# Kernel tuning notes

Measured on AMD Instinct MI355X. Metric: run time of the kernel, lower is better.

Reference implementation:

```python
import jax, jax.numpy as jnp
import numpy as np

B, K, D = 512, 20, 256


def _build_adjs(K):
    def tri(N):
        a = np.zeros((N, N), np.int32)
        a[0, 1] = a[1, 0] = 1
        a[0, 2] = a[2, 0] = 1
        a[1, 2] = a[2, 1] = 1
        return a
    adj1 = tri(3)
    adj2 = tri(3 + 3 * K)
    adj3 = tri(3 + 6 * K)
    for i in range(K):
        for c in range(3):
            adj2[c, 3 + c * K + i] = adj2[3 + c * K + i, c] = 2
            adj3[c, 3 + c * K + i] = adj3[3 + c * K + i, c] = 2
            adj3[c, 3 + 3 * K + c * K + i] = adj3[3 + 3 * K + c * K + i, c] = 3
    return jnp.asarray(adj1), jnp.asarray(adj2), jnp.asarray(adj3)

ADJ1, ADJ2, ADJ3 = _build_adjs(K)


def _rgat(h, adj, W, a_src, a_dst):
    # h: [B,N,F]; adj: [N,N] int relation labels (0 = no edge);
    # W: [R,F,E] per-relation projection; a_src/a_dst: [R,E] attention vecs.
    R = W.shape[0]
    Wh = jnp.einsum('bnf,rfe->brne', h, W)                      # [B,R,N,E]
    e = jax.nn.leaky_relu(
        jnp.einsum('brne,re->brn', Wh, a_src)[..., :, None]
        + jnp.einsum('brne,re->brn', Wh, a_dst)[..., None, :],
        negative_slope=0.2)                                     # [B,R,N,N]
    rel = jnp.arange(1, R + 1, dtype=jnp.int32)
    mask = (adj[None, :, :] == rel[:, None, None])[None]        # [1,R,N,N]
    alpha = jnp.where(mask, jax.nn.softmax(jnp.where(mask, e, -1e9), axis=-1), 0.0)
    return jax.nn.elu(jnp.einsum('brnm,brme->bne', alpha, Wh))  # [B,N,E]


def setup_inputs():
    key = jax.random.key(0)
    ks = jax.random.split(key, 40)
    n = lambda i, shp: jax.random.normal(ks[i], shp, dtype=jnp.float32)
    w = lambda i, shp: 0.02 * jax.random.normal(ks[i], shp, dtype=jnp.float32)
    inp = {
        'scene_tv': n(0, (B, 1, 1024)), 'face_tv': n(1, (B, 1, 1024)), 'text_tv': n(2, (B, 1, 2048)),
        'scene_refs': n(3, (B, K, 1024)), 'face_refs': n(4, (B, K, 1024)), 'text_refs': n(5, (B, K, 2048)),
        'scene_ra': n(6, (B, K, 1024)), 'face_ra': n(7, (B, K, 1024)), 'text_ra': n(8, (B, K, 1024)),
        'Ws1': w(9, (1024, D)), 'bs1': jnp.zeros((D,), jnp.float32),
        'Wf1': w(10, (1024, D)), 'bf1': jnp.zeros((D,), jnp.float32),
        'Wt1': w(11, (2048, D)), 'bt1': jnp.zeros((D,), jnp.float32),
        'G1W': w(12, (1, D, D)), 'G1as': w(13, (1, D)), 'G1ad': w(14, (1, D)),
        'Ws2': w(15, (1024, D)), 'bs2': jnp.zeros((D,), jnp.float32),
        'Wf2': w(16, (1024, D)), 'bf2': jnp.zeros((D,), jnp.float32),
        'Wt2': w(17, (2048, D)), 'bt2': jnp.zeros((D,), jnp.float32),
        'G2W': w(18, (2, D, D)), 'G2as': w(19, (2, D)), 'G2ad': w(20, (2, D)),
        'Ws3': w(21, (1024, D)), 'bs3': jnp.zeros((D,), jnp.float32),
        'Wf3': w(22, (1024, D)), 'bf3': jnp.zeros((D,), jnp.float32),
        'Wt3': w(23, (1024, D)), 'bt3': jnp.zeros((D,), jnp.float32),
        'G3W': w(24, (3, D, D)), 'G3as': w(25, (3, D)), 'G3ad': w(26, (3, D)),
    }
    return inp


def reference(scene_tv, face_tv, text_tv, scene_refs, face_refs, text_refs,
              scene_ra, face_ra, text_ra,
              Ws1, bs1, Wf1, bf1, Wt1, bt1, G1W, G1as, G1ad,
              Ws2, bs2, Wf2, bf2, Wt2, bt2, G2W, G2as, G2ad,
              Ws3, bs3, Wf3, bf3, Wt3, bt3, G3W, G3as, G3ad):
    # Stage 1: Basic_Emotion_Graph (3 nodes, 1 relation type)
    nodes1 = jnp.concatenate([scene_tv @ Ws1 + bs1,
                              face_tv @ Wf1 + bf1,
                              text_tv @ Wt1 + bt1], axis=1)      # [B,3,D]
    g1 = _rgat(nodes1, ADJ1, G1W, G1as, G1ad)
    # Stage 2: Indirect_Emotion_Extended_Graph (3+3K nodes, 2 relation types)
    nodes2 = jnp.concatenate([g1,
                              scene_refs @ Ws2 + bs2,
                              face_refs @ Wf2 + bf2,
                              text_refs @ Wt2 + bt2], axis=1)    # [B,3+3K,D]
    g2 = _rgat(nodes2, ADJ2, G2W, G2as, G2ad)
    # Stage 3: Direct_Emotion_Extended_Graph (3+6K nodes, 3 relation types)
    nodes3 = jnp.concatenate([g2,
                              scene_ra @ Ws3 + bs3,
                              face_ra @ Wf3 + bf3,
                              text_ra @ Wt3 + bt3], axis=1)      # [B,3+6K,D]
    return _rgat(nodes3, ADJ3, G3W, G3as, G3ad)
```

## Files before the change

### kernel.cpp

```cpp
#include <hip/hip_runtime.h>
#include <hip/hip_bf16.h>
#include <math.h>

typedef __bf16 bf16_t;
typedef __bf16 bf16x8 __attribute__((ext_vector_type(8)));
typedef __bf16 bf16x4 __attribute__((ext_vector_type(4)));
typedef float  floatx4 __attribute__((ext_vector_type(4)));

#define NB 512
#define DI 256

__device__ __forceinline__ float lrelu_f(float x){ return x >= 0.f ? x : 0.2f*x; }
__device__ __forceinline__ float elu_f(float x){ return x > 0.f ? x : expm1f(x); }

__global__ __launch_bounds__(256)
void detect_k(const void* __restrict__ probe, int* __restrict__ flag)
{
    __shared__ int cnt_s;
    if (threadIdx.x == 0) cnt_s = 0;
    __syncthreads();
    const unsigned short* u = (const unsigned short*)probe;
    int c = 0;
    for (int i = threadIdx.x; i < 16384; i += 256) {
        int e = (u[i] >> 7) & 0xFF;
        if (e >= 0x90) c++;
    }
    atomicAdd(&cnt_s, c);
    __syncthreads();
    if (threadIdx.x == 0) *flag = (cnt_s > 64) ? 1 : 0;
}

struct SCEnt { const void* s; bf16_t* d; int n; };
struct SCArgs { SCEnt e[16]; int cnt; };

__global__ __launch_bounds__(256)
void smallconv_k(SCArgs a, const int* __restrict__ flag)
{
    int isf = *flag;
    for (int k = 0; k < a.cnt; ++k) {
        int n = a.e[k].n;
        for (int i = threadIdx.x + blockIdx.x * 256; i < n; i += gridDim.x * 256) {
            float v = isf ? ((const float*)a.e[k].s)[i]
                          : (float)((const bf16_t*)a.e[k].s)[i];
            a.e[k].d[i] = (bf16_t)v;
        }
    }
}

struct TDesc { const void* W; size_t eoff; bf16_t* WT; int K; int tstart; };
struct TArgs { TDesc d[15]; int nd; };

__global__ __launch_bounds__(256)
void transpose_multi_k(TArgs ta, const int* __restrict__ flagp)
{
    __shared__ bf16_t tile[32][33];
    const int isf = *flagp;
    const int bx = blockIdx.x;
    int di = 0;
    while (di + 1 < ta.nd && bx >= ta.d[di + 1].tstart) ++di;
    const void* Wbase = ta.d[di].W;
    const size_t eoff = ta.d[di].eoff;
    bf16_t* WT        = ta.d[di].WT;
    const int K       = ta.d[di].K;
    const int ti      = bx - ta.d[di].tstart;
    const int tk      = K >> 5;
    const int kb      = (ti % tk) * 32;
    const int nb      = (ti / tk) * 32;
    const int tx = threadIdx.x & 31, ty = threadIdx.x >> 5;
    #pragma unroll
    for (int rr = 0; rr < 4; ++rr) {
        int r = ty + rr * 8;
        size_t idx = eoff + (size_t)(kb + r) * 256 + nb + tx;
        tile[r][tx] = isf ? (bf16_t)((const float*)Wbase)[idx]
                          : ((const bf16_t*)Wbase)[idx];
    }
    __syncthreads();
    #pragma unroll
    for (int rr = 0; rr < 4; ++rr) {
        int r = ty + rr * 8;
        WT[(size_t)(nb + r) * K + kb + tx] = tile[tx][r];
    }
}

#define BM 64
#define BN 64
#define BK 32
#define LST 40

struct GDesc {
    const void* A; const bf16_t* WT; const bf16_t* bias; bf16_t* out;
    int Kin, in_stride_b, in_off, rows_pb, a_is_ext, out_stride_b, out_off, mb_start;
};
struct GArgs { GDesc d[9]; int nd; };

__global__ __launch_bounds__(256)
void gemm_multi_k(GArgs ga, const int* __restrict__ flagp)
{
    __shared__ bf16_t As[BM * LST];
    __shared__ bf16_t Bs[BN * LST];

    const int bx = blockIdx.x;
    int di = 0;
    while (di + 1 < ga.nd && bx >= ga.d[di + 1].mb_start) ++di;

    const void*   A        = ga.d[di].A;
    const bf16_t* WT       = ga.d[di].WT;
    const bf16_t* bias     = ga.d[di].bias;
    bf16_t*       out      = ga.d[di].out;
    const int Kin          = ga.d[di].Kin;
    const int in_stride_b  = ga.d[di].in_stride_b;
    const int in_off       = ga.d[di].in_off;
    const int rows_pb      = ga.d[di].rows_pb;
    const int out_stride_b = ga.d[di].out_stride_b;
    const int out_off      = ga.d[di].out_off;
    const int a_fp32 = ga.d[di].a_is_ext ? *flagp : 0;

    const int t  = threadIdx.x;
    const int m0 = (bx - ga.d[di].mb_start) * BM;
    const int n0 = blockIdx.y * BN;

    const int s_row = t >> 2;
    const int s_col = (t & 3) * 8;

    const int g_row = m0 + s_row;
    const int b_idx = g_row / rows_pb;
    const int i_idx = g_row - b_idx * rows_pb;
    const size_t a_base = (size_t)(b_idx * in_stride_b + in_off + i_idx) * Kin + s_col;
    const bf16_t* w_ptr = WT + (size_t)(n0 + s_row) * Kin + s_col;

    const int wave = t >> 6;
    const int lane = t & 63;
    const int wr = (wave >> 1) * 32;
    const int wc = (wave & 1) * 32;
    const int lm = lane & 15;
    const int lk = (lane >> 4) * 8;

    floatx4 acc[2][2] = {};

    for (int kk = 0; kk < Kin; kk += BK) {
        bf16x8 av;
        if (a_fp32) {
            const float* ap = (const float*)A + a_base + kk;
            float4 f0 = *(const float4*)ap;
            float4 f1 = *(const float4*)(ap + 4);
            av[0] = (bf16_t)f0.x; av[1] = (bf16_t)f0.y;
            av[2] = (bf16_t)f0.z; av[3] = (bf16_t)f0.w;
            av[4] = (bf16_t)f1.x; av[5] = (bf16_t)f1.y;
            av[6] = (bf16_t)f1.z; av[7] = (bf16_t)f1.w;
        } else {
            av = *(const bf16x8*)((const bf16_t*)A + a_base + kk);
        }
        bf16x8 wv = *(const bf16x8*)(w_ptr + kk);
        *(bf16x8*)(&As[s_row * LST + s_col]) = av;
        *(bf16x8*)(&Bs[s_row * LST + s_col]) = wv;
        __syncthreads();

        bf16x8 af0 = *(const bf16x8*)(&As[(wr      + lm) * LST + lk]);
        bf16x8 af1 = *(const bf16x8*)(&As[(wr + 16 + lm) * LST + lk]);
        bf16x8 bf0 = *(const bf16x8*)(&Bs[(wc      + lm) * LST + lk]);
        bf16x8 bf1 = *(const bf16x8*)(&Bs[(wc + 16 + lm) * LST + lk]);

        acc[0][0] = __builtin_amdgcn_mfma_f32_16x16x32_bf16(af0, bf0, acc[0][0], 0, 0, 0);
        acc[0][1] = __builtin_amdgcn_mfma_f32_16x16x32_bf16(af0, bf1, acc[0][1], 0, 0, 0);
        acc[1][0] = __builtin_amdgcn_mfma_f32_16x16x32_bf16(af1, bf0, acc[1][0], 0, 0, 0);
        acc[1][1] = __builtin_amdgcn_mfma_f32_16x16x32_bf16(af1, bf1, acc[1][1], 0, 0, 0);
        __syncthreads();
    }

    const int q = lane >> 4;
    #pragma unroll
    for (int i = 0; i < 2; ++i)
      #pragma unroll
      for (int j = 0; j < 2; ++j)
        #pragma unroll
        for (int r = 0; r < 4; ++r) {
            int row = m0 + wr + i * 16 + q * 4 + r;
            int col = n0 + wc + j * 16 + lm;
            int bb = row / rows_pb;
            int ii = row - bb * rows_pb;
            float v = acc[i][j][r];
            if (bias) v += (float)bias[col];
            out[(size_t)(bb * out_stride_b + out_off + ii) * DI + col] = (bf16_t)v;
        }
}

struct SDesc { const bf16_t* Wh; const bf16_t* as_; const bf16_t* ad_;
               float* s; float* d; int bstart; };
struct SArgs { SDesc e[3]; int nd; };

__global__ __launch_bounds__(256)
void scores_multi_k(SArgs sa)
{
    const int bx = blockIdx.x;
    int di = 0;
    while (di + 1 < sa.nd && bx >= sa.e[di + 1].bstart) ++di;
    const bf16_t* Wh    = sa.e[di].Wh;
    const bf16_t* a_src = sa.e[di].as_;
    const bf16_t* a_dst = sa.e[di].ad_;
    float* src = sa.e[di].s;
    float* dst = sa.e[di].d;

    int wid  = (bx - sa.e[di].bstart) * 4 + (threadIdx.x >> 6);
    int lane = threadIdx.x & 63;
    bf16x4 wv = *(const bf16x4*)(Wh + (size_t)wid * DI + lane * 4);
    bf16x4 sv = *(const bf16x4*)(a_src + lane * 4);
    bf16x4 dv = *(const bf16x4*)(a_dst + lane * 4);
    float s = 0.f, d = 0.f;
    #pragma unroll
    for (int i = 0; i < 4; ++i) {
        float w = (float)wv[i];
        s += w * (float)sv[i];
        d += w * (float)dv[i];
    }
    #pragma unroll
    for (int off = 32; off > 0; off >>= 1) {
        s += __shfl_down(s, off);
        d += __shfl_down(d, off);
    }
    if (lane == 0) { src[wid] = s; dst[wid] = d; }
}

__device__ __forceinline__ float hub20(const bf16_t* __restrict__ Wh,
                                       const float* __restrict__ s,
                                       const float* __restrict__ d,
                                       int b, int c, int e)
{
    int base = b * 63 + 3 + c * 20;
    float ss = s[b * 63 + c];
    float ev[20], mx = -1e30f;
    #pragma unroll
    for (int i = 0; i < 20; ++i) { ev[i] = lrelu_f(ss + d[base + i]); mx = fmaxf(mx, ev[i]); }
    float sw = 0.f, acc = 0.f;
    #pragma unroll
    for (int i = 0; i < 20; ++i) {
        float w = expf(ev[i] - mx);
        sw  += w;
        acc += w * (float)Wh[(size_t)(base + i) * DI + e];
    }
    return acc / sw;
}

__device__ __forceinline__ float hub_tri(const bf16_t* __restrict__ Wh1,
                                         const float* __restrict__ s1,
                                         const float* __restrict__ d1,
                                         int b, int c, int e)
{
    int m0 = (c == 0) ? 1 : 0, m1 = (c == 2) ? 1 : 2;
    float ss = s1[b * 3 + c];
    float e0 = lrelu_f(ss + d1[b * 3 + m0]);
    float e1 = lrelu_f(ss + d1[b * 3 + m1]);
    float mx = fmaxf(e0, e1);
    float w0 = expf(e0 - mx), w1 = expf(e1 - mx);
    return (w0 * (float)Wh1[(size_t)(b * 3 + m0) * DI + e] +
            w1 * (float)Wh1[(size_t)(b * 3 + m1) * DI + e]) / (w0 + w1);
}

__global__ __launch_bounds__(256)
void agg1_k(const bf16_t* __restrict__ Wh1, const float* __restrict__ s1,
            const float* __restrict__ d1, bf16_t* __restrict__ nodes2)
{
    int blk = blockIdx.x;
    int b = blk / 3, n = blk - b * 3;
    int e = threadIdx.x;
    float v = hub_tri(Wh1, s1, d1, b, n, e);
    nodes2[(size_t)(b * 63 + n) * DI + e] = (bf16_t)elu_f(v);
}

__global__ __launch_bounds__(256)
void agg2_k(const bf16_t* __restrict__ Wh1, const bf16_t* __restrict__ Wh2,
            const float* __restrict__ s1, const float* __restrict__ d1,
            const float* __restrict__ s2, const float* __restrict__ d2,
            bf16_t* __restrict__ nodes3)
{
    int blk = blockIdx.x;
    int b = blk / 63, n = blk - b * 63;
    int e = threadIdx.x;
    float v;
    if (n >= 3) {
        int c = (n - 3) / 20;
        v = (float)Wh2[(size_t)(b * 63 + c) * DI + e];
    } else {
        v = hub_tri(Wh1, s1, d1, b, n, e) + hub20(Wh2, s2, d2, b, n, e);
    }
    nodes3[(size_t)(b * 123 + n) * DI + e] = (bf16_t)elu_f(v);
}

__global__ __launch_bounds__(256)
void agg3_k(const bf16_t* __restrict__ Wh1, const bf16_t* __restrict__ Wh2,
            const bf16_t* __restrict__ Wh3,
            const float* __restrict__ s1, const float* __restrict__ d1,
            const float* __restrict__ s2, const float* __restrict__ d2,
            const float* __restrict__ s3, const float* __restrict__ d3,
            void* __restrict__ out, const int* __restrict__ flagp)
{
    int isf = *flagp;
    int blk = blockIdx.x;
    int b = blk / 123, n = blk - b * 123;
    int e = threadIdx.x;
    float v;
    if (n >= 63) {
        int c = (n - 63) / 20;
        v = (float)Wh3[(size_t)(b * 63 + c) * DI + e];
    } else if (n >= 3) {
        int c = (n - 3) / 20;
        v = (float)Wh2[(size_t)(b * 63 + c) * DI + e];
    } else {
        v = hub_tri(Wh1, s1, d1, b, n, e)
          + hub20(Wh2, s2, d2, b, n, e)
          + hub20(Wh3, s3, d3, b, n, e);
    }
    float r = elu_f(v);
    size_t oi = (size_t)(b * 123 + n) * DI + e;
    if (isf) ((float*)out)[oi] = r;
    else     ((bf16_t*)out)[oi] = (bf16_t)r;
}

extern "C" void kernel_launch(void* const* d_in, const int* in_sizes, int n_in,
                              void* d_out, int out_size, void* d_ws, size_t ws_size,
                              hipStream_t stream)
{
    (void)in_sizes; (void)n_in; (void)out_size; (void)ws_size;
    const void *scene_tv=d_in[0], *face_tv=d_in[1], *text_tv=d_in[2],
               *scene_refs=d_in[3], *face_refs=d_in[4], *text_refs=d_in[5],
               *scene_ra=d_in[6], *face_ra=d_in[7], *text_ra=d_in[8],
               *Ws1=d_in[9],  *bs1=d_in[10], *Wf1=d_in[11], *bf1=d_in[12],
               *Wt1=d_in[13], *bt1=d_in[14],
               *G1W=d_in[15], *G1as=d_in[16], *G1ad=d_in[17],
               *Ws2=d_in[18], *bs2=d_in[19], *Wf2=d_in[20], *bf2=d_in[21],
               *Wt2=d_in[22], *bt2=d_in[23],
               *G2W=d_in[24], *G2as=d_in[25], *G2ad=d_in[26],
               *Ws3=d_in[27], *bs3=d_in[28], *Wf3=d_in[29], *bf3=d_in[30],
               *Wt3=d_in[31], *bt3=d_in[32],
               *G3W=d_in[33], *G3as=d_in[34], *G3ad=d_in[35];

    char* p = (char*)d_ws;
    auto carveB = [&](size_t elems) -> bf16_t* { bf16_t* r = (bf16_t*)p; p += ((elems*2 + 255) & ~(size_t)255); return r; };
    auto carveF = [&](size_t elems) -> float*  { float*  r = (float*)p;  p += ((elems*4 + 255) & ~(size_t)255); return r; };
    auto carveI = [&]() -> int* { int* r = (int*)p; p += 256; return r; };

    int* flag = carveI();

    bf16_t* Ws1T = carveB(1024*256); bf16_t* Wf1T = carveB(1024*256); bf16_t* Wt1T = carveB(2048*256);
    bf16_t* Ws2T = carveB(1024*256); bf16_t* Wf2T = carveB(1024*256); bf16_t* Wt2T = carveB(2048*256);
    bf16_t* Ws3T = carveB(1024*256); bf16_t* Wf3T = carveB(1024*256); bf16_t* Wt3T = carveB(1024*256);
    bf16_t* G1WT = carveB(256*256);
    bf16_t* G2WT = carveB(2*256*256);
    bf16_t* G3WT = carveB(3*256*256);

    bf16_t* cb[9];
    for (int i = 0; i < 9; ++i) cb[i] = carveB(256);
    bf16_t* a1s = carveB(256); bf16_t* a1d = carveB(256);
    bf16_t* a2s = carveB(512); bf16_t* a2d = carveB(512);
    bf16_t* a3s = carveB(768); bf16_t* a3d = carveB(768);

    bf16_t* nodes1 = carveB((size_t)NB*3*DI);
    bf16_t* nodes2 = carveB((size_t)NB*63*DI);
    bf16_t* nodes3 = carveB((size_t)NB*123*DI);
    bf16_t* Wh1    = carveB((size_t)NB*3*DI);
    bf16_t* Wh2    = carveB((size_t)NB*63*DI);
    bf16_t* Wh3    = carveB((size_t)NB*63*DI);
    float* s1s = carveF(NB*3);  float* s1d = carveF(NB*3);
    float* s2s = carveF(NB*63); float* s2d = carveF(NB*63);
    float* s3s = carveF(NB*63); float* s3d = carveF(NB*63);

    detect_k<<<1, 256, 0, stream>>>(Ws1, flag);

    SCArgs sca;
    const void* ssrc[15] = { bs1, bf1, bt1, bs2, bf2, bt2, bs3, bf3, bt3,
                             G1as, G1ad, G2as, G2ad, G3as, G3ad };
    bf16_t* sdst[15] = { cb[0],cb[1],cb[2],cb[3],cb[4],cb[5],cb[6],cb[7],cb[8],
                         a1s, a1d, a2s, a2d, a3s, a3d };
    int sn[15] = { 256,256,256,256,256,256,256,256,256, 256,256,512,512,768,768 };
    for (int i = 0; i < 15; ++i) { sca.e[i].s = ssrc[i]; sca.e[i].d = sdst[i]; sca.e[i].n = sn[i]; }
    sca.cnt = 15;
    smallconv_k<<<1, 256, 0, stream>>>(sca, flag);

    TArgs ta; ta.nd = 0; int tcum = 0;
    auto addT = [&](const void* W, size_t eoff, bf16_t* WT, int K) {
        ta.d[ta.nd].W = W; ta.d[ta.nd].eoff = eoff; ta.d[ta.nd].WT = WT;
        ta.d[ta.nd].K = K; ta.d[ta.nd].tstart = tcum;
        tcum += (K / 32) * 8; ta.nd++;
    };
    addT(Ws1, 0, Ws1T, 1024); addT(Wf1, 0, Wf1T, 1024); addT(Wt1, 0, Wt1T, 2048);
    addT(Ws2, 0, Ws2T, 1024); addT(Wf2, 0, Wf2T, 1024); addT(Wt2, 0, Wt2T, 2048);
    addT(Ws3, 0, Ws3T, 1024); addT(Wf3, 0, Wf3T, 1024); addT(Wt3, 0, Wt3T, 1024);
    addT(G1W, 0,      G1WT,          256);
    addT(G2W, 0,      G2WT,          256); addT(G2W, 65536,  G2WT + 65536,  256);
    addT(G3W, 0,      G3WT,          256); addT(G3W, 65536,  G3WT + 65536,  256);
    addT(G3W, 131072, G3WT + 131072, 256);
    transpose_multi_k<<<tcum, 256, 0, stream>>>(ta, flag);

    auto addG = [](GArgs& A, int& cum, const void* Ain, int Kin, int isb, int ioff,
                   int rpb, int ext, const bf16_t* WT, const bf16_t* bias,
                   bf16_t* out, int osb, int ooff, int M) {
        GDesc& g = A.d[A.nd];
        g.A = Ain; g.WT = WT; g.bias = bias; g.out = out;
        g.Kin = Kin; g.in_stride_b = isb; g.in_off = ioff; g.rows_pb = rpb;
        g.a_is_ext = ext; g.out_stride_b = osb; g.out_off = ooff; g.mb_start = cum;
        cum += M / 64; A.nd++;
    };

    GArgs pg; pg.nd = 0; int pc = 0;
    addG(pg, pc, scene_tv,   1024,  1, 0,  1, 1, Ws1T, cb[0], nodes1,   3,   0, NB);
    addG(pg, pc, face_tv,    1024,  1, 0,  1, 1, Wf1T, cb[1], nodes1,   3,   1, NB);
    addG(pg, pc, text_tv,    2048,  1, 0,  1, 1, Wt1T, cb[2], nodes1,   3,   2, NB);
    addG(pg, pc, scene_refs, 1024, 20, 0, 20, 1, Ws2T, cb[3], nodes2,  63,   3, NB*20);
    addG(pg, pc, face_refs,  1024, 20, 0, 20, 1, Wf2T, cb[4], nodes2,  63,  23, NB*20);
    addG(pg, pc, text_refs,  2048, 20, 0, 20, 1, Wt2T, cb[5], nodes2,  63,  43, NB*20);
    addG(pg, pc, scene_ra,   1024, 20, 0, 20, 1, Ws3T, cb[6], nodes3, 123,  63, NB*20);
    addG(pg, pc, face_ra,    1024, 20, 0, 20, 1, Wf3T, cb[7], nodes3, 123,  83, NB*20);
    addG(pg, pc, text_ra,    1024, 20, 0, 20, 1, Wt3T, cb[8], nodes3, 123, 103, NB*20);
    gemm_multi_k<<<dim3(pc, 4), 256, 0, stream>>>(pg, flag);

    GArgs g1; g1.nd = 0; int c1 = 0;
    addG(g1, c1, nodes1, 256, 3, 0, 3, 0, G1WT, nullptr, Wh1, 3, 0, NB*3);
    gemm_multi_k<<<dim3(c1, 4), 256, 0, stream>>>(g1, flag);

    SArgs s1a; s1a.nd = 1;
    s1a.e[0].Wh = Wh1; s1a.e[0].as_ = a1s; s1a.e[0].ad_ = a1d;
    s1a.e[0].s = s1s; s1a.e[0].d = s1d; s1a.e[0].bstart = 0;
    scores_multi_k<<<NB*3/4, 256, 0, stream>>>(s1a);
    agg1_k<<<NB*3, 256, 0, stream>>>(Wh1, s1s, s1d, nodes2);

    GArgs g2; g2.nd = 0; int c2 = 0;
    addG(g2, c2, nodes2, 256, 63, 0,  3, 0, G2WT,         nullptr, Wh1,  3, 0, NB*3);
    addG(g2, c2, nodes2, 256, 63, 0, 63, 0, G2WT + 65536, nullptr, Wh2, 63, 0, NB*63);
    gemm_multi_k<<<dim3(c2, 4), 256, 0, stream>>>(g2, flag);

    SArgs s2a; s2a.nd = 2;
    s2a.e[0].Wh = Wh1; s2a.e[0].as_ = a2s;       s2a.e[0].ad_ = a2d;
    s2a.e[0].s = s1s;  s2a.e[0].d = s1d;         s2a.e[0].bstart = 0;
    s2a.e[1].Wh = Wh2; s2a.e[1].as_ = a2s + 256; s2a.e[1].ad_ = a2d + 256;
    s2a.e[1].s = s2s;  s2a.e[1].d = s2d;         s2a.e[1].bstart = NB*3/4;
    scores_multi_k<<<NB*3/4 + NB*63/4, 256, 0, stream>>>(s2a);
    agg2_k<<<NB*63, 256, 0, stream>>>(Wh1, Wh2, s1s, s1d, s2s, s2d, nodes3);

    GArgs g3; g3.nd = 0; int c3 = 0;
    addG(g3, c3, nodes3, 256, 123,  0,  3, 0, G3WT,          nullptr, Wh1,  3, 0, NB*3);
    addG(g3, c3, nodes3, 256, 123,  0, 63, 0, G3WT + 65536,  nullptr, Wh2, 63, 0, NB*63);
    addG(g3, c3, nodes3, 256, 123,  0,  3, 0, G3WT + 131072, nullptr, Wh3, 63, 0, NB*3);
    addG(g3, c3, nodes3, 256, 123, 63, 60, 0, G3WT + 131072, nullptr, Wh3, 63, 3, NB*60);
    gemm_multi_k<<<dim3(c3, 4), 256, 0, stream>>>(g3, flag);

    SArgs s3a; s3a.nd = 3;
    s3a.e[0].Wh = Wh1; s3a.e[0].as_ = a3s;       s3a.e[0].ad_ = a3d;
    s3a.e[0].s = s1s;  s3a.e[0].d = s1d;         s3a.e[0].bstart = 0;
    s3a.e[1].Wh = Wh2; s3a.e[1].as_ = a3s + 256; s3a.e[1].ad_ = a3d + 256;
    s3a.e[1].s = s2s;  s3a.e[1].d = s2d;         s3a.e[1].bstart = NB*3/4;
    s3a.e[2].Wh = Wh3; s3a.e[2].as_ = a3s + 512; s3a.e[2].ad_ = a3d + 512;
    s3a.e[2].s = s3s;  s3a.e[2].d = s3d;         s3a.e[2].bstart = NB*3/4 + NB*63/4;
    scores_multi_k<<<NB*3/4 + 2*(NB*63/4), 256, 0, stream>>>(s3a);
    agg3_k<<<NB*123, 256, 0, stream>>>(Wh1, Wh2, Wh3, s1s, s1d, s2s, s2d, s3s, s3d,
                                       d_out, flag);
}
```

Before: 650.1 us.

## Widen GEMM tile to full 256-column output per block

Each GEMM block now computes all 256 output columns for its 64 rows instead of a 64-column slice, so the grid's y dimension goes away. The A tile, including the fp32-to-bf16 conversion of the large external inputs, is read once rather than four times, and each wave issues 16 MFMAs per k-step. The cost is more accumulator registers per thread (64 floats), a larger shared-memory B tile, and a quarter as many blocks, which may lower occupancy and latency hiding.

New measurement: 632.0 us. -2.8%, faster.

```diff
diff --git a/kernel.cpp b/kernel.cpp
--- a/kernel.cpp
+++ b/kernel.cpp
@@ -83,7 +83,7 @@
 }
 
 #define BM 64
-#define BN 64
+#define BNF 256
 #define BK 32
 #define LST 40
 
@@ -97,7 +97,7 @@
 void gemm_multi_k(GArgs ga, const int* __restrict__ flagp)
 {
     __shared__ bf16_t As[BM * LST];
-    __shared__ bf16_t Bs[BN * LST];
+    __shared__ bf16_t Bs[BNF * LST];
 
     const int bx = blockIdx.x;
     int di = 0;
@@ -117,25 +117,24 @@
 
     const int t  = threadIdx.x;
     const int m0 = (bx - ga.d[di].mb_start) * BM;
-    const int n0 = blockIdx.y * BN;
 
     const int s_row = t >> 2;
     const int s_col = (t & 3) * 8;
-
     const int g_row = m0 + s_row;
     const int b_idx = g_row / rows_pb;
     const int i_idx = g_row - b_idx * rows_pb;
     const size_t a_base = (size_t)(b_idx * in_stride_b + in_off + i_idx) * Kin + s_col;
-    const bf16_t* w_ptr = WT + (size_t)(n0 + s_row) * Kin + s_col;
+
+    const bf16_t* w_ptr = WT + (size_t)t * Kin;
 
     const int wave = t >> 6;
     const int lane = t & 63;
     const int wr = (wave >> 1) * 32;
-    const int wc = (wave & 1) * 32;
+    const int wc = (wave & 1) * 128;
     const int lm = lane & 15;
     const int lk = (lane >> 4) * 8;
 
-    floatx4 acc[2][2] = {};
+    floatx4 acc[2][8] = {};
 
     for (int kk = 0; kk < Kin; kk += BK) {
         bf16x8 av;
@@ -150,20 +149,25 @@
         } else {
             av = *(const bf16x8*)((const bf16_t*)A + a_base + kk);
         }
-        bf16x8 wv = *(const bf16x8*)(w_ptr + kk);
+        bf16x8 wv0 = *(const bf16x8*)(w_ptr + kk);
+        bf16x8 wv1 = *(const bf16x8*)(w_ptr + kk + 8);
+        bf16x8 wv2 = *(const bf16x8*)(w_ptr + kk + 16);
+        bf16x8 wv3 = *(const bf16x8*)(w_ptr + kk + 24);
         *(bf16x8*)(&As[s_row * LST + s_col]) = av;
-        *(bf16x8*)(&Bs[s_row * LST + s_col]) = wv;
+        *(bf16x8*)(&Bs[t * LST +  0]) = wv0;
+        *(bf16x8*)(&Bs[t * LST +  8]) = wv1;
+        *(bf16x8*)(&Bs[t * LST + 16]) = wv2;
+        *(bf16x8*)(&Bs[t * LST + 24]) = wv3;
         __syncthreads();
 
         bf16x8 af0 = *(const bf16x8*)(&As[(wr      + lm) * LST + lk]);
         bf16x8 af1 = *(const bf16x8*)(&As[(wr + 16 + lm) * LST + lk]);
-        bf16x8 bf0 = *(const bf16x8*)(&Bs[(wc      + lm) * LST + lk]);
-        bf16x8 bf1 = *(const bf16x8*)(&Bs[(wc + 16 + lm) * LST + lk]);
-
-        acc[0][0] = __builtin_amdgcn_mfma_f32_16x16x32_bf16(af0, bf0, acc[0][0], 0, 0, 0);
-        acc[0][1] = __builtin_amdgcn_mfma_f32_16x16x32_bf16(af0, bf1, acc[0][1], 0, 0, 0);
-        acc[1][0] = __builtin_amdgcn_mfma_f32_16x16x32_bf16(af1, bf0, acc[1][0], 0, 0, 0);
-        acc[1][1] = __builtin_amdgcn_mfma_f32_16x16x32_bf16(af1, bf1, acc[1][1], 0, 0, 0);
+        #pragma unroll
+        for (int j = 0; j < 8; ++j) {
+            bf16x8 bfj = *(const bf16x8*)(&Bs[(wc + j * 16 + lm) * LST + lk]);
+            acc[0][j] = __builtin_amdgcn_mfma_f32_16x16x32_bf16(af0, bfj, acc[0][j], 0, 0, 0);
+            acc[1][j] = __builtin_amdgcn_mfma_f32_16x16x32_bf16(af1, bfj, acc[1][j], 0, 0, 0);
+        }
         __syncthreads();
     }
 
@@ -171,11 +175,11 @@
     #pragma unroll
     for (int i = 0; i < 2; ++i)
       #pragma unroll
-      for (int j = 0; j < 2; ++j)
+      for (int j = 0; j < 8; ++j)
         #pragma unroll
         for (int r = 0; r < 4; ++r) {
             int row = m0 + wr + i * 16 + q * 4 + r;
-            int col = n0 + wc + j * 16 + lm;
+            int col = wc + j * 16 + lm;
             int bb = row / rows_pb;
             int ii = row - bb * rows_pb;
             float v = acc[i][j][r];
@@ -410,11 +414,11 @@
     addG(pg, pc, scene_ra,   1024, 20, 0, 20, 1, Ws3T, cb[6], nodes3, 123,  63, NB*20);
     addG(pg, pc, face_ra,    1024, 20, 0, 20, 1, Wf3T, cb[7], nodes3, 123,  83, NB*20);
     addG(pg, pc, text_ra,    1024, 20, 0, 20, 1, Wt3T, cb[8], nodes3, 123, 103, NB*20);
-    gemm_multi_k<<<dim3(pc, 4), 256, 0, stream>>>(pg, flag);
+    gemm_multi_k<<<pc, 256, 0, stream>>>(pg, flag);
 
     GArgs g1; g1.nd = 0; int c1 = 0;
     addG(g1, c1, nodes1, 256, 3, 0, 3, 0, G1WT, nullptr, Wh1, 3, 0, NB*3);
-    gemm_multi_k<<<dim3(c1, 4), 256, 0, stream>>>(g1, flag);
+    gemm_multi_k<<<c1, 256, 0, stream>>>(g1, flag);
 
     SArgs s1a; s1a.nd = 1;
     s1a.e[0].Wh = Wh1; s1a.e[0].as_ = a1s; s1a.e[0].ad_ = a1d;
@@ -425,7 +429,7 @@
     GArgs g2; g2.nd = 0; int c2 = 0;
     addG(g2, c2, nodes2, 256, 63, 0,  3, 0, G2WT,         nullptr, Wh1,  3, 0, NB*3);
     addG(g2, c2, nodes2, 256, 63, 0, 63, 0, G2WT + 65536, nullptr, Wh2, 63, 0, NB*63);
-    gemm_multi_k<<<dim3(c2, 4), 256, 0, stream>>>(g2, flag);
+    gemm_multi_k<<<c2, 256, 0, stream>>>(g2, flag);
 
     SArgs s2a; s2a.nd = 2;
     s2a.e[0].Wh = Wh1; s2a.e[0].as_ = a2s;       s2a.e[0].ad_ = a2d;
@@ -440,7 +444,7 @@
     addG(g3, c3, nodes3, 256, 123,  0, 63, 0, G3WT + 65536,  nullptr, Wh2, 63, 0, NB*63);
     addG(g3, c3, nodes3, 256, 123,  0,  3, 0, G3WT + 131072, nullptr, Wh3, 63, 0, NB*3);
     addG(g3, c3, nodes3, 256, 123, 63, 60, 0, G3WT + 131072, nullptr, Wh3, 63, 3, NB*60);
-    gemm_multi_k<<<dim3(c3, 4), 256, 0, stream>>>(g3, flag);
+    gemm_multi_k<<<c3, 256, 0, stream>>>(g3, flag);
 
     SArgs s3a; s3a.nd = 3;
     s3a.e[0].Wh = Wh1; s3a.e[0].as_ = a3s;       s3a.e[0].ad_ = a3d;
```
